# Kernel tuning notes

Measured on AMD Instinct MI355X. Metric: run time of the kernel, lower is better.

Reference implementation:

```python
import jax, jax.numpy as jnp
import numpy as np
import math

N_NODES = 64000
N_GRAPHS = 512
HIDDEN = 128
CLUSTERS = 10
NUM_FILTER = 16
N_CLASSES = 2
S_HID = math.ceil((HIDDEN + CLUSTERS) / 2)  # 69
P_HID = 8


def _mlp2(x, w1, b1, w2, b2):
    # 2-layer MLP: Linear -> ReLU -> Linear (matches MLP(2, in, hid, out))
    return jax.nn.relu(x @ w1 + b1) @ w2 + b2


def setup_inputs() -> dict:
    key = jax.random.key(0)
    ks = jax.random.split(key, 12)
    # node embeddings (output of get_emb)
    H_all = jax.random.normal(ks[0], (N_NODES, HIDDEN), dtype=jnp.float32)
    # graph indicator: 125 nodes per graph, sorted (as produced by batching)
    batch = jnp.repeat(jnp.arange(N_GRAPHS, dtype=jnp.int32), N_NODES // N_GRAPHS)
    targets = jax.random.randint(ks[1], (N_GRAPHS,), 0, N_CLASSES, dtype=jnp.int32)
    s = 0.05
    # S_mlp: hidden -> S_HID -> clusters
    w1 = jax.random.normal(ks[2], (HIDDEN, S_HID), dtype=jnp.float32) * s
    b1 = jnp.zeros((S_HID,), dtype=jnp.float32)
    w2 = jax.random.normal(ks[3], (S_HID, CLUSTERS), dtype=jnp.float32) * s
    b2 = jnp.zeros((CLUSTERS,), dtype=jnp.float32)
    # final: hidden*clusters -> 2
    wf = jax.random.normal(ks[4], (HIDDEN * CLUSTERS, N_CLASSES), dtype=jnp.float32) * s
    bf = jnp.zeros((N_CLASSES,), dtype=jnp.float32)
    # prototype_features_MLP: hidden -> 8 -> num_graph_filter
    p1 = jax.random.normal(ks[5], (HIDDEN, P_HID), dtype=jnp.float32) * s
    pb1 = jnp.zeros((P_HID,), dtype=jnp.float32)
    p2 = jax.random.normal(ks[6], (P_HID, NUM_FILTER), dtype=jnp.float32) * s
    pb2 = jnp.zeros((NUM_FILTER,), dtype=jnp.float32)
    # correlation parameters (initialized like the torch module)
    corr_inter = jax.nn.softmax(jax.random.uniform(ks[7], (N_CLASSES, NUM_FILTER)), axis=0)
    corr_intra = jax.nn.softmax(jax.random.uniform(ks[8], (N_CLASSES, NUM_FILTER)), axis=1)
    return {"H_all": H_all, "batch": batch, "targets": targets,
            "w1": w1, "b1": b1, "w2": w2, "b2": b2,
            "wf": wf, "bf": bf,
            "p1": p1, "pb1": pb1, "p2": p2, "pb2": pb2,
            "corr_inter": corr_inter, "corr_intra": corr_intra}


def reference(H_all, batch, targets, w1, b1, w2, b2, wf, bf,
              p1, pb1, p2, pb2, corr_inter, corr_intra):
    # per-node soft cluster assignment  [N, C]
    S_all = jax.nn.softmax(_mlp2(H_all, w1, b1, w2, b2), axis=-1)
    # segment matmul E_g = S_g^T @ H_g  -> [B, C, D] via segment-reduced outer products
    outer = S_all[:, :, None] * H_all[:, None, :]  # [N, C, D]
    E_all = jax.ops.segment_sum(outer, batch, num_segments=N_GRAPHS)
    B = E_all.shape[0]
    pred1 = E_all.reshape(B, -1) @ wf + bf  # dropout off (eval)
    p = jax.nn.softmax(pred1, axis=-1)
    # multinomial sample from pred_softmax (no grad)
    key = jax.random.key(42)
    sample = jax.random.categorical(key, jnp.log(jax.lax.stop_gradient(p) + 1e-12), axis=-1)
    ind_positive_sample = sample == targets
    oh = jax.nn.one_hot(sample, N_CLASSES, dtype=p.dtype)
    epsilon = jax.lax.stop_gradient(jnp.where(oh != 0, 1.0 - p, -p))
    sample_cat_oh = p + epsilon  # straight-through one-hot
    Q = jax.nn.softmax(_mlp2(E_all, p1, pb1, p2, pb2), axis=-1)  # [B, C, F]
    correlation = jax.nn.softmax(corr_inter, axis=0) * jax.nn.softmax(corr_intra, axis=1)  # [2, F]
    correlation_mask = sample_cat_oh @ correlation  # [B, F]
    feature_mask = jnp.sum(Q * correlation_mask[:, None, :], axis=-1)  # [B, C]
    E_masked = feature_mask[:, :, None] * E_all  # einsum('bi,bij->bij')
    pred2 = E_masked.reshape(B, -1) @ wf + bf
    return (pred1, pred2, ind_positive_sample, S_all, E_all, Q)
```

## Files before the change

kernel.cpp:

```cpp
#include <hip/hip_runtime.h>

#define NN 64000
#define NG 512
#define NPG 125
#define DIM 128
#define NC 10
#define SHID 69
#define NF 16
#define PHID 8
#define ELPAD 132

#define OFF_PRED1 0
#define OFF_PRED2 1024
#define OFF_IND   2048
#define OFF_S     2560
#define OFF_E     642560
#define OFF_Q     1297920

__device__ __forceinline__ unsigned rotl32(unsigned x, int r) {
    return (x << r) | (x >> (32 - r));
}

__device__ __forceinline__ void threefry_0_42(unsigned x0, unsigned x1,
                                              unsigned& o0, unsigned& o1) {
    const unsigned k0 = 0u, k1 = 42u;
    const unsigned k2 = k0 ^ k1 ^ 0x1BD11BDAu;
    unsigned ks[3] = {k0, k1, k2};
    const int R0[4] = {13, 15, 26, 6};
    const int R1[4] = {17, 29, 16, 24};
    x0 += k0; x1 += k1;
    #pragma unroll
    for (int i = 0; i < 5; i++) {
        const int* R = (i & 1) ? R1 : R0;
        #pragma unroll
        for (int r = 0; r < 4; r++) {
            x0 += x1;
            x1 = rotl32(x1, R[r]);
            x1 ^= x0;
        }
        x0 += ks[(i + 1) % 3];
        x1 += ks[(i + 2) % 3] + (unsigned)(i + 1);
    }
    o0 = x0; o1 = x1;
}

__device__ __forceinline__ unsigned random_bits_partitionable(unsigned i) {
    unsigned o0, o1;
    threefry_0_42(0u, i, o0, o1);
    return o0 ^ o1;
}

__device__ __forceinline__ float gumbel_from_bits(unsigned bits) {
    float f = __uint_as_float((bits >> 9) | 0x3f800000u) - 1.0f;
    if (f <= 0.0f) f = 1.1754943508222875e-38f;
    return -logf(-logf(f));
}

#define R24(M) M(0) M(1) M(2) M(3) M(4) M(5) M(6) M(7) M(8) M(9) M(10) M(11) \
               M(12) M(13) M(14) M(15) M(16) M(17) M(18) M(19) M(20) M(21) M(22) M(23)
#define R10(M) M(0) M(1) M(2) M(3) M(4) M(5) M(6) M(7) M(8) M(9)

__global__ __launch_bounds__(192, 3) void k_node_mlp(
    const float* __restrict__ H, const float* __restrict__ w1,
    const float* __restrict__ b1, const float* __restrict__ w2,
    const float* __restrict__ b2, float* __restrict__ S) {
    __shared__ float red[NC * 3 * 64];
    int tid = threadIdx.x;
    int lane = tid & 63;
    int wu = __builtin_amdgcn_readfirstlane(tid >> 6);
    int jbase = wu * 24;
    int node = blockIdx.x * 64 + lane;

    const float4* H4 = (const float4*)(H + (size_t)node * DIM);
    const float* w1s = w1 + jbase;

    #define DT(i) float t##i = 0.0f;
    R24(DT)
    #undef DT

    #define F(i) t##i = fmaf(hk, wr[i], t##i);
    #pragma unroll 2
    for (int k4 = 0; k4 < 32; k4++) {
        float4 h4 = H4[k4];
        { float hk = h4.x; const float* wr = w1s + (k4 * 4 + 0) * SHID; R24(F) }
        { float hk = h4.y; const float* wr = w1s + (k4 * 4 + 1) * SHID; R24(F) }
        { float hk = h4.z; const float* wr = w1s + (k4 * 4 + 2) * SHID; R24(F) }
        { float hk = h4.w; const float* wr = w1s + (k4 * 4 + 3) * SHID; R24(F) }
    }
    #undef F

    #define DL(c) float lg##c = 0.0f;
    R10(DL)
    #undef DL
    #define L2(i) { \
        int jv = jbase + (i); \
        int jx = (jv < SHID) ? jv : (SHID - 1); \
        float tr = (jv < SHID) ? fmaxf(t##i + b1[jx], 0.0f) : 0.0f; \
        const float* w2r = w2 + jx * NC; \
        lg0 = fmaf(tr, w2r[0], lg0); lg1 = fmaf(tr, w2r[1], lg1); \
        lg2 = fmaf(tr, w2r[2], lg2); lg3 = fmaf(tr, w2r[3], lg3); \
        lg4 = fmaf(tr, w2r[4], lg4); lg5 = fmaf(tr, w2r[5], lg5); \
        lg6 = fmaf(tr, w2r[6], lg6); lg7 = fmaf(tr, w2r[7], lg7); \
        lg8 = fmaf(tr, w2r[8], lg8); lg9 = fmaf(tr, w2r[9], lg9); }
    R24(L2)
    #undef L2

    #define ST(c) red[(c) * 192 + wu * 64 + lane] = lg##c;
    R10(ST)
    #undef ST
    __syncthreads();

    if (wu == 0) {
        #define LD(c) float s##c = red[(c) * 192 + lane] + red[(c) * 192 + 64 + lane] \
                                 + red[(c) * 192 + 128 + lane] + b2[c];
        R10(LD)
        #undef LD
        float m = fmaxf(fmaxf(fmaxf(s0, s1), fmaxf(s2, s3)),
                        fmaxf(fmaxf(fmaxf(s4, s5), fmaxf(s6, s7)), fmaxf(s8, s9)));
        float e0 = expf(s0 - m), e1 = expf(s1 - m), e2 = expf(s2 - m),
              e3 = expf(s3 - m), e4 = expf(s4 - m), e5 = expf(s5 - m),
              e6 = expf(s6 - m), e7 = expf(s7 - m), e8 = expf(s8 - m),
              e9 = expf(s9 - m);
        float ssum = ((e0 + e1) + (e2 + e3)) + ((e4 + e5) + (e6 + e7)) + (e8 + e9);
        float inv = 1.0f / ssum;
        float2* Sp2 = (float2*)(S + (size_t)node * NC);
        Sp2[0] = make_float2(e0 * inv, e1 * inv);
        Sp2[1] = make_float2(e2 * inv, e3 * inv);
        Sp2[2] = make_float2(e4 * inv, e5 * inv);
        Sp2[3] = make_float2(e6 * inv, e7 * inv);
        Sp2[4] = make_float2(e8 * inv, e9 * inv);
    }
}

__global__ __launch_bounds__(512, 2) void k_E_tail(
    const float* __restrict__ H, const float* __restrict__ S,
    const float* __restrict__ wf, const float* __restrict__ bf,
    const int* __restrict__ targets,
    const float* __restrict__ p1, const float* __restrict__ pb1,
    const float* __restrict__ p2, const float* __restrict__ pb2,
    const float* __restrict__ ci, const float* __restrict__ cr,
    float* __restrict__ E, float* __restrict__ pred1, float* __restrict__ pred2,
    float* __restrict__ ind, float* __restrict__ Q) {
    __shared__ float Sl[128 * NC];
    __shared__ float Epart[3 * 128 * NC];
    __shared__ __align__(16) float El[NC * ELPAD];
    __shared__ float fmbuf[NC];
    int g = blockIdx.x, tid = threadIdx.x;

    const float* Sg = S + (size_t)g * NPG * NC;
    for (int i = tid; i < 128 * NC; i += 512) Sl[i] = (i < NPG * NC) ? Sg[i] : 0.0f;
    __syncthreads();

    int q = tid >> 7;
    int d = tid & 127;
    const float* Hg = H + (size_t)g * NPG * DIM + d;

    #define DECLA(c) float a##c = 0.f;
    R10(DECLA)
    #undef DECLA
    int n0 = q * 32;
    #pragma unroll 8
    for (int i = 0; i < 32; i++) {
        int n = n0 + i;
        int nh = min(n, NPG - 1);
        float h = Hg[(size_t)nh * DIM];
        #define ACC(c) a##c = fmaf(Sl[n * NC + c], h, a##c);
        R10(ACC)
        #undef ACC
    }
    if (q > 0) {
        float* ep = &Epart[(q - 1) * 128 * NC + d * NC];
        #define STP(c) ep[c] = a##c;
        R10(STP)
        #undef STP
    }
    __syncthreads();
    if (q == 0) {
        const float* e1p = &Epart[d * NC];
        const float* e2p = &Epart[128 * NC + d * NC];
        const float* e3p = &Epart[2 * 128 * NC + d * NC];
        float* Eo = E + (size_t)g * (NC * DIM) + d;
        #define CMB(c) { a##c += e1p[c] + e2p[c] + e3p[c]; \
                         El[c * ELPAD + d] = a##c; Eo[c * DIM] = a##c; }
        R10(CMB)
        #undef CMB
    }
    __syncthreads();

    const float2* wf2 = (const float2*)wf;
    int l = tid;
    int samp = 0;
    float corr_lf = 0.f;

    if (tid < 64) {
        if (l < 32) {
            int i = l >> 4, f = l & 15;
            float a = ci[f], b = ci[NF + f];
            float mm = fmaxf(a, b);
            float ea = expf(a - mm), eb = expf(b - mm);
            float inter = expf(ci[i * NF + f] - mm) / (ea + eb);
            float mi = -1e30f;
            for (int j = 0; j < NF; j++) mi = fmaxf(mi, cr[i * NF + j]);
            float ri = 0.f;
            for (int j = 0; j < NF; j++) ri += expf(cr[i * NF + j] - mi);
            float intra = expf(cr[i * NF + f] - mi) / ri;
            corr_lf = inter * intra;
        }

        float a0 = 0.f, a1 = 0.f;
        #pragma unroll
        for (int i = 0; i < 20; i++) {
            int idx = i * 64 + l;
            float e = El[(idx >> 7) * ELPAD + (idx & 127)];
            float2 w = wf2[idx];
            a0 = fmaf(e, w.x, a0);
            a1 = fmaf(e, w.y, a1);
        }
        #pragma unroll
        for (int off = 32; off > 0; off >>= 1) {
            a0 += __shfl_down(a0, off);
            a1 += __shfl_down(a1, off);
        }
        if (l == 0) {
            float y0 = a0 + bf[0], y1 = a1 + bf[1];
            pred1[g * 2] = y0;
            pred1[g * 2 + 1] = y1;
            float m = fmaxf(y0, y1);
            float e0 = expf(y0 - m), e1 = expf(y1 - m), s = e0 + e1;
            float p0 = e0 / s, pp1 = e1 / s;
            float g0 = gumbel_from_bits(random_bits_partitionable(2 * g));
            float g1 = gumbel_from_bits(random_bits_partitionable(2 * g + 1));
            float l0 = logf(p0 + 1e-12f) + g0;
            float l1 = logf(pp1 + 1e-12f) + g1;
            samp = (l1 > l0) ? 1 : 0;
            ind[g] = (samp == targets[g]) ? 1.0f : 0.0f;
        }
        samp = __shfl(samp, 0);

        if (l < 40) {
            int p = l >> 2, s = l & 3;
            float ua = pb1[2 * s], ub = pb1[2 * s + 1];
            const float4* E4 = (const float4*)&El[p * ELPAD];
            #pragma unroll 4
            for (int k4 = 0; k4 < 32; k4++) {
                float4 e4 = E4[k4];
                float es[4] = {e4.x, e4.y, e4.z, e4.w};
                #pragma unroll
                for (int kk = 0; kk < 4; kk++) {
                    int k = k4 * 4 + kk;
                    ua = fmaf(es[kk], p1[k * PHID + 2 * s], ua);
                    ub = fmaf(es[kk], p1[k * PHID + 2 * s + 1], ub);
                }
            }
            ua = fmaxf(ua, 0.f);
            ub = fmaxf(ub, 0.f);
            float v[NF];
            #pragma unroll
            for (int f = 0; f < NF; f++) {
                v[f] = pb2[f] * 0.25f;
                v[f] = fmaf(ua, p2[(2 * s) * NF + f], v[f]);
                v[f] = fmaf(ub, p2[(2 * s + 1) * NF + f], v[f]);
            }
            #pragma unroll
            for (int f = 0; f < NF; f++) {
                v[f] += __shfl_xor(v[f], 1);
                v[f] += __shfl_xor(v[f], 2);
            }
            float m = v[0];
            #pragma unroll
            for (int f = 1; f < NF; f++) m = fmaxf(m, v[f]);
            float ssum = 0.f, qv[NF];
            #pragma unroll
            for (int f = 0; f < NF; f++) { qv[f] = expf(v[f] - m); ssum += qv[f]; }
            float inv = 1.0f / ssum;
            #pragma unroll
            for (int f = 0; f < NF; f++) qv[f] *= inv;
            float* Qo = Q + ((size_t)g * NC + p) * NF;
            ((float4*)Qo)[s] = make_float4(qv[s * 4], qv[s * 4 + 1], qv[s * 4 + 2], qv[s * 4 + 3]);
            float fmv = 0.f;
            #pragma unroll
            for (int f = 0; f < NF; f++) {
                float cv = __shfl(corr_lf, samp * NF + f);
                fmv = fmaf(qv[f], cv, fmv);
            }
            if (s == 0) fmbuf[p] = fmv;
        }
    }
    __syncthreads();

    if (tid < 64) {
        float b0 = 0.f, b1acc = 0.f;
        #pragma unroll
        for (int i = 0; i < 20; i++) {
            int idx = i * 64 + l;
            float e = El[(idx >> 7) * ELPAD + (idx & 127)] * fmbuf[idx >> 7];
            float2 w = wf2[idx];
            b0 = fmaf(e, w.x, b0);
            b1acc = fmaf(e, w.y, b1acc);
        }
        #pragma unroll
        for (int off = 32; off > 0; off >>= 1) {
            b0 += __shfl_down(b0, off);
            b1acc += __shfl_down(b1acc, off);
        }
        if (l == 0) {
            pred2[g * 2] = b0 + bf[0];
            pred2[g * 2 + 1] = b1acc + bf[1];
        }
    }
}

extern "C" void kernel_launch(void* const* d_in, const int* in_sizes, int n_in,
                              void* d_out, int out_size, void* d_ws, size_t ws_size,
                              hipStream_t stream) {
    const float* H       = (const float*)d_in[0];
    const int*   targets = (const int*)d_in[2];
    const float* w1      = (const float*)d_in[3];
    const float* b1      = (const float*)d_in[4];
    const float* w2      = (const float*)d_in[5];
    const float* b2      = (const float*)d_in[6];
    const float* wf      = (const float*)d_in[7];
    const float* bf      = (const float*)d_in[8];
    const float* p1      = (const float*)d_in[9];
    const float* pb1     = (const float*)d_in[10];
    const float* p2      = (const float*)d_in[11];
    const float* pb2     = (const float*)d_in[12];
    const float* ci      = (const float*)d_in[13];
    const float* cr      = (const float*)d_in[14];

    float* out   = (float*)d_out;
    float* pred1 = out + OFF_PRED1;
    float* pred2 = out + OFF_PRED2;
    float* ind   = out + OFF_IND;
    float* S     = out + OFF_S;
    float* E     = out + OFF_E;
    float* Q     = out + OFF_Q;

    k_node_mlp<<<NN / 64, 192, 0, stream>>>(H, w1, b1, w2, b2, S);
    k_E_tail<<<NG, 512, 0, stream>>>(H, S, wf, bf, targets, p1, pb1, p2, pb2,
                                     ci, cr, E, pred1, pred2, ind, Q);
}
```

Measured before the change: 138.5 us.

## Register-tile node MLP first layer with w1 staged in shared memory

The first MLP layer changes from each thread computing 24 hidden units for one node, with w1 read from global memory, to a 4-node by 5-hidden-unit register tile per thread. w1 is zero-padded to 80 columns and staged once per block in LDS. The hidden activations then pass through LDS for a 4-way split second layer before the softmax. The aim is more FMA work per weight and H load. The cost is a per-block w1 staging loop, about 60KB of LDS, and extra synchronisation, which may reduce occupancy.

```diff
diff --git a/kernel.cpp b/kernel.cpp
--- a/kernel.cpp
+++ b/kernel.cpp
@@ -8,6 +8,7 @@
 #define SHID 69
 #define NF 16
 #define PHID 8
+#define WP 80
 #define ELPAD 132
 
 #define OFF_PRED1 0
@@ -56,63 +57,80 @@
     return -logf(-logf(f));
 }
 
-#define R24(M) M(0) M(1) M(2) M(3) M(4) M(5) M(6) M(7) M(8) M(9) M(10) M(11) \
-               M(12) M(13) M(14) M(15) M(16) M(17) M(18) M(19) M(20) M(21) M(22) M(23)
 #define R10(M) M(0) M(1) M(2) M(3) M(4) M(5) M(6) M(7) M(8) M(9)
 
-__global__ __launch_bounds__(192, 3) void k_node_mlp(
+__global__ __launch_bounds__(256, 2) void k_node_mlp(
     const float* __restrict__ H, const float* __restrict__ w1,
     const float* __restrict__ b1, const float* __restrict__ w2,
     const float* __restrict__ b2, float* __restrict__ S) {
-    __shared__ float red[NC * 3 * 64];
+    __shared__ __align__(16) float Ws[DIM * WP];
+    __shared__ __align__(16) float Ts[64 * WP];
+    __shared__ float Ps[64 * 40];
     int tid = threadIdx.x;
-    int lane = tid & 63;
-    int wu = __builtin_amdgcn_readfirstlane(tid >> 6);
-    int jbase = wu * 24;
-    int node = blockIdx.x * 64 + lane;
-
-    const float4* H4 = (const float4*)(H + (size_t)node * DIM);
-    const float* w1s = w1 + jbase;
-
-    #define DT(i) float t##i = 0.0f;
-    R24(DT)
-    #undef DT
-
-    #define F(i) t##i = fmaf(hk, wr[i], t##i);
-    #pragma unroll 2
+
+    for (int i = tid; i < DIM * WP; i += 256) {
+        int k = i / WP, j = i - k * WP;
+        Ws[i] = (j < SHID) ? w1[k * SHID + j] : 0.0f;
+    }
+    __syncthreads();
+
+    int ty = tid >> 4, tx = tid & 15;
+    const float* Hp = H + ((size_t)blockIdx.x * 64 + ty * 4) * DIM;
+
+    float acc[4][5] = {};
     for (int k4 = 0; k4 < 32; k4++) {
-        float4 h4 = H4[k4];
-        { float hk = h4.x; const float* wr = w1s + (k4 * 4 + 0) * SHID; R24(F) }
-        { float hk = h4.y; const float* wr = w1s + (k4 * 4 + 1) * SHID; R24(F) }
-        { float hk = h4.z; const float* wr = w1s + (k4 * 4 + 2) * SHID; R24(F) }
-        { float hk = h4.w; const float* wr = w1s + (k4 * 4 + 3) * SHID; R24(F) }
-    }
-    #undef F
-
-    #define DL(c) float lg##c = 0.0f;
-    R10(DL)
-    #undef DL
-    #define L2(i) { \
-        int jv = jbase + (i); \
-        int jx = (jv < SHID) ? jv : (SHID - 1); \
-        float tr = (jv < SHID) ? fmaxf(t##i + b1[jx], 0.0f) : 0.0f; \
-        const float* w2r = w2 + jx * NC; \
-        lg0 = fmaf(tr, w2r[0], lg0); lg1 = fmaf(tr, w2r[1], lg1); \
-        lg2 = fmaf(tr, w2r[2], lg2); lg3 = fmaf(tr, w2r[3], lg3); \
-        lg4 = fmaf(tr, w2r[4], lg4); lg5 = fmaf(tr, w2r[5], lg5); \
-        lg6 = fmaf(tr, w2r[6], lg6); lg7 = fmaf(tr, w2r[7], lg7); \
-        lg8 = fmaf(tr, w2r[8], lg8); lg9 = fmaf(tr, w2r[9], lg9); }
-    R24(L2)
-    #undef L2
-
-    #define ST(c) red[(c) * 192 + wu * 64 + lane] = lg##c;
-    R10(ST)
-    #undef ST
-    __syncthreads();
-
-    if (wu == 0) {
-        #define LD(c) float s##c = red[(c) * 192 + lane] + red[(c) * 192 + 64 + lane] \
-                                 + red[(c) * 192 + 128 + lane] + b2[c];
+        float hk[4][4];
+        #pragma unroll
+        for (int i = 0; i < 4; i++) {
+            float4 v = *(const float4*)(Hp + i * DIM + k4 * 4);
+            hk[i][0] = v.x; hk[i][1] = v.y; hk[i][2] = v.z; hk[i][3] = v.w;
+        }
+        #pragma unroll
+        for (int kk = 0; kk < 4; kk++) {
+            float w[5];
+            #pragma unroll
+            for (int u = 0; u < 5; u++) w[u] = Ws[(k4 * 4 + kk) * WP + tx * 5 + u];
+            #pragma unroll
+            for (int i = 0; i < 4; i++) {
+                #pragma unroll
+                for (int u = 0; u < 5; u++)
+                    acc[i][u] = fmaf(hk[i][kk], w[u], acc[i][u]);
+            }
+        }
+    }
+
+    #pragma unroll
+    for (int u = 0; u < 5; u++) {
+        int j = tx * 5 + u;
+        float bj = (j < SHID) ? b1[j] : 0.0f;
+        #pragma unroll
+        for (int i = 0; i < 4; i++) {
+            float tr = fmaxf(acc[i][u] + bj, 0.0f);
+            Ts[(ty * 4 + i) * WP + j] = (j < SHID) ? tr : 0.0f;
+        }
+    }
+    __syncthreads();
+
+    {
+        int n = tid & 63, q = tid >> 6;
+        float lg[NC] = {};
+        for (int jj = 0; jj < 18; jj++) {
+            int j = q * 18 + jj;
+            int jx = (j < SHID) ? j : (SHID - 1);
+            float tr = Ts[n * WP + j];
+            const float* w2r = w2 + jx * NC;
+            #pragma unroll
+            for (int c = 0; c < NC; c++) lg[c] = fmaf(tr, w2r[c], lg[c]);
+        }
+        #pragma unroll
+        for (int c = 0; c < NC; c++) Ps[n * 40 + q * NC + c] = lg[c];
+    }
+    __syncthreads();
+
+    if (tid < 64) {
+        int n = tid;
+        const float* pr = &Ps[n * 40];
+        #define LD(c) float s##c = pr[c] + pr[10 + c] + pr[20 + c] + pr[30 + c] + b2[c];
         R10(LD)
         #undef LD
         float m = fmaxf(fmaxf(fmaxf(s0, s1), fmaxf(s2, s3)),
@@ -123,7 +141,7 @@
               e9 = expf(s9 - m);
         float ssum = ((e0 + e1) + (e2 + e3)) + ((e4 + e5) + (e6 + e7)) + (e8 + e9);
         float inv = 1.0f / ssum;
-        float2* Sp2 = (float2*)(S + (size_t)node * NC);
+        float2* Sp2 = (float2*)(S + ((size_t)blockIdx.x * 64 + n) * NC);
         Sp2[0] = make_float2(e0 * inv, e1 * inv);
         Sp2[1] = make_float2(e2 * inv, e3 * inv);
         Sp2[2] = make_float2(e4 * inv, e5 * inv);
@@ -336,7 +354,7 @@
     float* E     = out + OFF_E;
     float* Q     = out + OFF_Q;
 
-    k_node_mlp<<<NN / 64, 192, 0, stream>>>(H, w1, b1, w2, b2, S);
+    k_node_mlp<<<NN / 64, 256, 0, stream>>>(H, w1, b1, w2, b2, S);
     k_E_tail<<<NG, 512, 0, stream>>>(H, S, wf, bf, targets, p1, pb1, p2, pb2,
                                      ci, cr, E, pred1, pred2, ind, Q);
 }
```

Result: slower. 160.7 us (+16.0%).
